# Performance work log

Hardware: AMD Instinct MI355X
Metric: run time of the kernel (lower is better)

## Reference

```python
import jax, jax.numpy as jnp
import numpy as np

B, N, G, M = 16, 8192, 512, 32
ENC = 384   # encoder_dims
TRD = 384   # trans_dim (must equal ENC due to cls-pos concat)
EPS = 1e-5


def _fps(xyz, n_samples):
    # farthest point sampling: xyz [B,N,3] -> idx [B,n_samples] int32
    b, n, _ = xyz.shape
    def body(carry, _):
        dists, farthest = carry                       # [B,N], [B]
        centroid = jnp.take_along_axis(xyz, farthest[:, None, None], axis=1)  # [B,1,3]
        d = jnp.sum((xyz - centroid) ** 2, -1)        # [B,N]
        dists = jnp.minimum(dists, d)
        nxt = jnp.argmax(dists, -1).astype(jnp.int32)
        return (dists, nxt), farthest
    init = (jnp.full((b, n), 1e10, xyz.dtype), jnp.zeros((b,), jnp.int32))
    _, idxs = jax.lax.scan(body, init, None, length=n_samples)
    return idxs.T                                     # [B,n_samples]


def _group(pts):
    # FPS centers + kNN neighborhoods, neighborhood recentered on its center
    fps_idx = _fps(pts, G)                                    # [B,G]
    center = jax.vmap(lambda p, i: p[i])(pts, fps_idx)        # [B,G,3]
    d2 = jnp.sum((center[:, :, None, :] - pts[:, None, :, :]) ** 2, -1)  # [B,G,N]
    _, knn_idx = jax.lax.top_k(-d2, M)                        # [B,G,M]
    nbhd = jax.vmap(lambda p, i: p[i])(pts, knn_idx)          # [B,G,M,3]
    nbhd = nbhd - center[:, :, None, :]
    return nbhd, center


def _bn(x, g, b, m, v):
    return (x - m) * jax.lax.rsqrt(v + EPS) * g + b


def _forward(pts, W1, b1, g1, be1, m1, v1, W2, b2,
             W3, b3, g2, be2, m2, v2, W4, b4,
             Wp1, bp1, Wp2, bp2, cls_pos):
    nbhd, center = _group(pts)                                # [B,G,M,3], [B,G,3]
    # Encoder (Point-MAE, BN in eval mode)
    f = jnp.einsum('bgmc,cd->bgmd', nbhd, W1) + b1            # [B,G,M,128]
    f = jax.nn.relu(_bn(f, g1, be1, m1, v1))
    f = jnp.einsum('bgmc,cd->bgmd', f, W2) + b2               # [B,G,M,256]
    fg = jnp.max(f, axis=2, keepdims=True)                    # [B,G,1,256]
    f = jnp.concatenate([jnp.broadcast_to(fg, f.shape), f], -1)  # [B,G,M,512]
    f = jnp.einsum('bgmc,cd->bgmd', f, W3) + b3
    f = jax.nn.relu(_bn(f, g2, be2, m2, v2))
    f = jnp.einsum('bgmc,cd->bgmd', f, W4) + b4               # [B,G,M,ENC]
    x = jnp.max(f, axis=2)                                    # [B,G,ENC]
    # pos embed MLP on centers
    pos = jax.nn.gelu(center @ Wp1 + bp1) @ Wp2 + bp2         # [B,G,TRD]
    cls = jnp.broadcast_to(cls_pos, (pts.shape[0], 1, ENC))
    pos = jnp.concatenate([cls, pos], axis=1)                 # [B,G+1,TRD]
    return x, pos


def setup_inputs() -> dict:
    key = jax.random.key(0)
    ks = jax.random.split(key, 20)
    nrm = lambda k, s, sc: jax.random.normal(k, s, jnp.float32) * sc
    uni = lambda k, s: jax.random.uniform(k, s, jnp.float32, 0.5, 1.5)
    return {
        'pts': jax.random.normal(ks[0], (B, N, 3), jnp.float32),
        'W1': nrm(ks[1], (3, 128), 0.1), 'b1': jnp.zeros((128,), jnp.float32),
        'g1': uni(ks[2], (128,)), 'be1': nrm(ks[3], (128,), 0.1),
        'm1': nrm(ks[4], (128,), 0.1), 'v1': uni(ks[5], (128,)),
        'W2': nrm(ks[6], (128, 256), 0.05), 'b2': jnp.zeros((256,), jnp.float32),
        'W3': nrm(ks[7], (512, 512), 0.04), 'b3': jnp.zeros((512,), jnp.float32),
        'g2': uni(ks[8], (512,)), 'be2': nrm(ks[9], (512,), 0.1),
        'm2': nrm(ks[10], (512,), 0.1), 'v2': uni(ks[11], (512,)),
        'W4': nrm(ks[12], (512, ENC), 0.04), 'b4': jnp.zeros((ENC,), jnp.float32),
        'Wp1': nrm(ks[13], (3, 128), 0.1), 'bp1': jnp.zeros((128,), jnp.float32),
        'Wp2': nrm(ks[14], (128, TRD), 0.08), 'bp2': jnp.zeros((TRD,), jnp.float32),
        'cls_pos': nrm(ks[15], (1, 1, ENC), 0.02),
    }


def reference(pts, W1, b1, g1, be1, m1, v1, W2, b2, W3, b3, g2, be2, m2, v2,
              W4, b4, Wp1, bp1, Wp2, bp2, cls_pos):
    return _forward(pts, W1, b1, g1, be1, m1, v1, W2, b2, W3, b3, g2, be2,
                    m2, v2, W4, b4, Wp1, bp1, Wp2, bp2, cls_pos)
```

## Files before the change

### kernel.cpp

```cpp
#include <hip/hip_runtime.h>

typedef _Float16 f16;
typedef _Float16 f16x8 __attribute__((ext_vector_type(8)));
typedef float    f32x4 __attribute__((ext_vector_type(4)));

#define NB   16
#define NP   8192
#define NG   512
#define NM   32
#define ENC  384
#define NROWS (NB * NG * NM)

__device__ __forceinline__ void gl_lds16(const void* g, void* l) {
  __builtin_amdgcn_global_load_lds((const __attribute__((address_space(1))) unsigned int*)g,
                                   (__attribute__((address_space(3))) unsigned int*)l, 16, 0, 0);
}

__device__ __forceinline__ unsigned long long kmax(unsigned long long a, unsigned long long b) {
  return a > b ? a : b;
}
__device__ __forceinline__ unsigned long long kmin(unsigned long long a, unsigned long long b) {
  return a < b ? a : b;
}

template <int CTRL>
__device__ __forceinline__ unsigned long long dpp_kmax(unsigned long long k) {
  int lo = (int)(unsigned)(k & 0xFFFFFFFFull);
  int hi = (int)(unsigned)(k >> 32);
  int olo = __builtin_amdgcn_update_dpp(lo, lo, CTRL, 0xF, 0xF, false);
  int ohi = __builtin_amdgcn_update_dpp(hi, hi, CTRL, 0xF, 0xF, false);
  unsigned long long o = ((unsigned long long)(unsigned)ohi << 32) | (unsigned)olo;
  return kmax(k, o);
}
template <int CTRL>
__device__ __forceinline__ unsigned long long dpp_kmin(unsigned long long k) {
  int lo = (int)(unsigned)(k & 0xFFFFFFFFull);
  int hi = (int)(unsigned)(k >> 32);
  int olo = __builtin_amdgcn_update_dpp(lo, lo, CTRL, 0xF, 0xF, false);
  int ohi = __builtin_amdgcn_update_dpp(hi, hi, CTRL, 0xF, 0xF, false);
  unsigned long long o = ((unsigned long long)(unsigned)ohi << 32) | (unsigned)olo;
  return kmin(k, o);
}
__device__ __forceinline__ unsigned long long swz16_kmax(unsigned long long k) {
  int lo = (int)(unsigned)(k & 0xFFFFFFFFull);
  int hi = (int)(unsigned)(k >> 32);
  int olo = __builtin_amdgcn_ds_swizzle(lo, 0x401F);
  int ohi = __builtin_amdgcn_ds_swizzle(hi, 0x401F);
  unsigned long long o = ((unsigned long long)(unsigned)ohi << 32) | (unsigned)olo;
  return kmax(k, o);
}
__device__ __forceinline__ unsigned long long swz16_kmin(unsigned long long k) {
  int lo = (int)(unsigned)(k & 0xFFFFFFFFull);
  int hi = (int)(unsigned)(k >> 32);
  int olo = __builtin_amdgcn_ds_swizzle(lo, 0x401F);
  int ohi = __builtin_amdgcn_ds_swizzle(hi, 0x401F);
  unsigned long long o = ((unsigned long long)(unsigned)ohi << 32) | (unsigned)olo;
  return kmin(k, o);
}

#define DPP_QUAD_XOR1 0xB1
#define DPP_QUAD_XOR2 0x4E
#define DPP_HALF_MIRR 0x141
#define DPP_ROW_MIRR  0x140

__global__ __launch_bounds__(512) void fps_kernel(const float* __restrict__ pts,
                                                  float* __restrict__ centers) {
#pragma clang fp contract(off)
  const int b = blockIdx.x;
  const float* pb = pts + (size_t)b * NP * 3;
  const int t = threadIdx.x;
  const int lane = t & 63, wid = t >> 6;
  __shared__ float spx[NP], spy[NP], spz[NP];
  __shared__ unsigned long long swk[2][16];
  float px[16], py[16], pz[16], dd[16];
#pragma unroll
  for (int i = 0; i < 16; ++i) {
    int idx = t + i * 512;
    float x = pb[idx * 3 + 0], y = pb[idx * 3 + 1], z = pb[idx * 3 + 2];
    px[i] = x; py[i] = y; pz[i] = z; dd[i] = 1e10f;
    spx[idx] = x; spy[idx] = y; spz[idx] = z;
  }
  __syncthreads();
  float cx = spx[0], cy = spy[0], cz = spz[0];
  for (int g = 0; g < NG; ++g) {
    if (t == 0) {
      float* c = centers + ((size_t)b * NG + g) * 3;
      c[0] = cx; c[1] = cy; c[2] = cz;
    }
    float best = -1.0f; int bslot = 0;
#pragma unroll
    for (int i = 0; i < 16; ++i) {
      float dx = __fsub_rn(px[i], cx);
      float dy = __fsub_rn(py[i], cy);
      float dz = __fsub_rn(pz[i], cz);
      float d  = __fadd_rn(__fadd_rn(__fmul_rn(dx, dx), __fmul_rn(dy, dy)), __fmul_rn(dz, dz));
      dd[i] = fminf(dd[i], d);
      if (dd[i] > best) { best = dd[i]; bslot = i; }
    }
    int bidx = t + bslot * 512;
    unsigned long long key =
        ((unsigned long long)__float_as_uint(best) << 13) | (unsigned)(8191 - bidx);
    key = dpp_kmax<DPP_QUAD_XOR1>(key);
    key = dpp_kmax<DPP_QUAD_XOR2>(key);
    key = dpp_kmax<DPP_HALF_MIRR>(key);
    key = dpp_kmax<DPP_ROW_MIRR>(key);
    key = swz16_kmax(key);
    const int p = g & 1;
    if ((lane & 31) == 0) swk[p][wid * 2 + (lane >> 5)] = key;
    __syncthreads();
    unsigned long long k2 = swk[p][lane & 15];
    k2 = dpp_kmax<DPP_QUAD_XOR1>(k2);
    k2 = dpp_kmax<DPP_QUAD_XOR2>(k2);
    k2 = dpp_kmax<DPP_HALF_MIRR>(k2);
    k2 = dpp_kmax<DPP_ROW_MIRR>(k2);
    int widx = 8191 - (int)(k2 & 0x1FFFull);
    cx = spx[widx]; cy = spy[widx]; cz = spz[widx];
  }
}

__global__ __launch_bounds__(256) void knn_kernel(const float* __restrict__ pts,
                                                  const float* __restrict__ centers,
                                                  int* __restrict__ knn_idx) {
#pragma clang fp contract(off)
  const int gg = blockIdx.x;
  const int b = gg >> 9;
  const float* pb = pts + (size_t)b * NP * 3;
  const float* c = centers + (size_t)gg * 3;
  const float cx = c[0], cy = c[1], cz = c[2];
  __shared__ unsigned long long swk[2][8];
  const int t = threadIdx.x, lane = t & 63, wid = t >> 6;
  float d[32];
  float lmin = 3e38f; int lidx = 0;
#pragma unroll
  for (int i = 0; i < 32; ++i) {
    int idx = i * 256 + t;
    float dx = __fsub_rn(cx, pb[idx * 3 + 0]);
    float dy = __fsub_rn(cy, pb[idx * 3 + 1]);
    float dz = __fsub_rn(cz, pb[idx * 3 + 2]);
    d[i] = __fadd_rn(__fadd_rn(__fmul_rn(dx, dx), __fmul_rn(dy, dy)), __fmul_rn(dz, dz));
    if (d[i] < lmin) { lmin = d[i]; lidx = idx; }
  }
  int* outp = knn_idx + (size_t)gg * NM;
  for (int r = 0; r < NM; ++r) {
    unsigned long long key =
        ((unsigned long long)__float_as_uint(lmin) << 13) | (unsigned)lidx;
    key = dpp_kmin<DPP_QUAD_XOR1>(key);
    key = dpp_kmin<DPP_QUAD_XOR2>(key);
    key = dpp_kmin<DPP_HALF_MIRR>(key);
    key = dpp_kmin<DPP_ROW_MIRR>(key);
    key = swz16_kmin(key);
    const int p = r & 1;
    if ((lane & 31) == 0) swk[p][wid * 2 + (lane >> 5)] = key;
    __syncthreads();
    unsigned long long k2 = swk[p][lane & 7];
    k2 = dpp_kmin<DPP_QUAD_XOR1>(k2);
    k2 = dpp_kmin<DPP_QUAD_XOR2>(k2);
    k2 = dpp_kmin<DPP_HALF_MIRR>(k2);
    int i0 = (int)(k2 & 0x1FFFull);
    if (t == 0) outp[r] = i0;
    if ((i0 & 255) == t) {
      int slot = i0 >> 8;
      lmin = 3e38f; lidx = 0;
#pragma unroll
      for (int i = 0; i < 32; ++i) {
        float di = (i == slot) ? 3e38f : d[i];
        d[i] = di;
        if (di < lmin) { lmin = di; lidx = i * 256 + t; }
      }
    }
  }
}

__global__ void quant_kernel(const float* __restrict__ W2, const float* __restrict__ W3,
                             const float* __restrict__ W4, const float* __restrict__ Wp2,
                             const float* __restrict__ b1, const float* __restrict__ g1,
                             const float* __restrict__ be1, const float* __restrict__ m1,
                             const float* __restrict__ v1, const float* __restrict__ g2,
                             const float* __restrict__ be2, const float* __restrict__ m2,
                             const float* __restrict__ v2,
                             f16* __restrict__ W2T, f16* __restrict__ W3aT,
                             f16* __restrict__ W3bT, f16* __restrict__ W4T,
                             f16* __restrict__ Wp2T,
                             float* __restrict__ s1, float* __restrict__ sh1,
                             float* __restrict__ s2, float* __restrict__ sh2) {
  int i = blockIdx.x * 256 + threadIdx.x;
  if (i < 32768) { int n = i >> 7, k = i & 127; W2T[i] = (f16)W2[(size_t)k * 256 + n]; return; }
  i -= 32768;
  if (i < 131072) { int n = i >> 8, k = i & 255; W3aT[i] = (f16)W3[(size_t)k * 512 + n]; return; }
  i -= 131072;
  if (i < 131072) { int n = i >> 8, k = i & 255; W3bT[i] = (f16)W3[(size_t)(256 + k) * 512 + n]; return; }
  i -= 131072;
  if (i < 196608) { int n = i >> 9, k = i & 511; W4T[i] = (f16)W4[(size_t)k * 384 + n]; return; }
  i -= 196608;
  if (i < 49152) { int n = i >> 7, k = i & 127; Wp2T[i] = (f16)Wp2[(size_t)k * 384 + n]; return; }
  i -= 49152;
  if (i < 128) {
    float s = g1[i] * rsqrtf(v1[i] + 1e-5f);
    s1[i] = s; sh1[i] = (b1[i] - m1[i]) * s + be1[i];
    return;
  }
  i -= 128;
  if (i < 512) {
    float s = g2[i] * rsqrtf(v2[i] + 1e-5f);
    s2[i] = s; sh2[i] = be2[i] - m2[i] * s;
    return;
  }
}

template <int WRITE_F2>
__global__ __launch_bounds__(256) void l2f_kernel(const float* __restrict__ pts,
                                                  const float* __restrict__ centers,
                                                  const int* __restrict__ knn_idx,
                                                  const float* __restrict__ W1,
                                                  const float* __restrict__ s1,
                                                  const float* __restrict__ sh1,
                                                  const f16* __restrict__ W2T,
                                                  const float* __restrict__ b2,
                                                  f16* __restrict__ fg,
                                                  f16* __restrict__ f2, int grow0) {
  __shared__ __align__(16) f16 sF1[128 * 128];
  __shared__ float snb[128][3];
  const int t = threadIdx.x, lane = t & 63, wid = t >> 6;
  const int wr = wid >> 1, wc = wid & 1;
  const int l15 = lane & 15, lhi = lane >> 4;
  const int grow = grow0 + blockIdx.x * 128;
  const int y = blockIdx.y;

  if (t < 128) {
    int row = grow + t;
    int gg = row >> 5;
    int b = gg >> 9;
    int idx = knn_idx[(size_t)gg * NM + (row & 31)];
    const float* p = pts + ((size_t)b * NP + idx) * 3;
    const float* c = centers + (size_t)gg * 3;
    snb[t][0] = p[0] - c[0];
    snb[t][1] = p[1] - c[1];
    snb[t][2] = p[2] - c[2];
  }
  __syncthreads();
  {
    int row = t >> 1, c0 = (t & 1) * 64;
    float nx = snb[row][0], ny = snb[row][1], nz = snb[row][2];
    int sw = (row & 7) << 4;
#pragma unroll
    for (int cc = 0; cc < 64; cc += 8) {
      f16x8 v;
#pragma unroll
      for (int j = 0; j < 8; ++j) {
        int c = c0 + cc + j;
        float a = nx * W1[c] + ny * W1[128 + c] + nz * W1[256 + c];
        a = a * s1[c] + sh1[c];
        v[j] = (f16)fmaxf(a, 0.0f);
      }
      *(f16x8*)((char*)sF1 + row * 256 + (((c0 + cc) * 2) ^ sw)) = v;
    }
  }
  __syncthreads();

  f32x4 acc[4][4];
#pragma unroll
  for (int m = 0; m < 4; ++m)
#pragma unroll
    for (int n = 0; n < 4; ++n) acc[m][n] = (f32x4){0.f, 0.f, 0.f, 0.f};

  const f16* Wb = W2T + (size_t)(y * 128) * 128;
#pragma unroll
  for (int ks = 0; ks < 4; ++ks) {
    f16x8 af[4], bf[4];
#pragma unroll
    for (int m = 0; m < 4; ++m) {
      int row = wr * 64 + m * 16 + l15;
      af[m] = *(const f16x8*)((const char*)sF1 + row * 256 + ((ks * 64 + lhi * 16) ^ ((row & 7) << 4)));
    }
#pragma unroll
    for (int n = 0; n < 4; ++n) {
      int nr = wc * 64 + n * 16 + l15;
      bf[n] = *(const f16x8*)(Wb + (size_t)nr * 128 + ks * 32 + lhi * 8);
    }
#pragma unroll
    for (int m = 0; m < 4; ++m)
#pragma unroll
      for (int n = 0; n < 4; ++n)
        acc[m][n] = __builtin_amdgcn_mfma_f32_16x16x32_f16(af[m], bf[n], acc[m][n], 0, 0, 0);
  }

  float bias[4];
#pragma unroll
  for (int n = 0; n < 4; ++n) bias[n] = b2[y * 128 + wc * 64 + n * 16 + l15];
#pragma unroll
  for (int p = 0; p < 2; ++p) {
#pragma unroll
    for (int n = 0; n < 4; ++n) {
      float v = acc[2 * p][n][0];
#pragma unroll
      for (int i = 1; i < 4; ++i) v = fmaxf(v, acc[2 * p][n][i]);
#pragma unroll
      for (int i = 0; i < 4; ++i) v = fmaxf(v, acc[2 * p + 1][n][i]);
      v = fmaxf(v, __shfl_xor(v, 16));
      v = fmaxf(v, __shfl_xor(v, 32));
      if (lhi == 0)
        fg[(size_t)((grow >> 5) + wr * 2 + p) * 256 + y * 128 + wc * 64 + n * 16 + l15] =
            (f16)(v + bias[n]);
    }
  }

  if (WRITE_F2) {
    __syncthreads();
    f16* sF2 = sF1;
#pragma unroll
    for (int n = 0; n < 4; ++n) {
      int col = wc * 64 + n * 16 + l15;
#pragma unroll
      for (int m = 0; m < 4; ++m)
#pragma unroll
        for (int i = 0; i < 4; ++i) {
          int row = wr * 64 + m * 16 + lhi * 4 + i;
          sF2[row * 128 + col] = (f16)(acc[m][n][i] + bias[n]);
        }
    }
    __syncthreads();
#pragma unroll
    for (int ch = 0; ch < 8; ++ch) {
      int off = ch * 4096 + t * 16;
      int row = off >> 8, cb = off & 255;
      *(uint4*)((char*)f2 + (size_t)(blockIdx.x * 128 + row) * 512 + y * 256 + cb) =
          *(const uint4*)((const char*)sF2 + off);
    }
  }
}

template <int K, int EPI>
__global__ __launch_bounds__(256) void gemm128_kernel(const f16* __restrict__ A,
                                                      const f16* __restrict__ BT,
                                                      float* __restrict__ outF32,
                                                      f16* __restrict__ outF16,
                                                      const float* __restrict__ e0,
                                                      const float* __restrict__ e1,
                                                      const float* __restrict__ e2,
                                                      int NTOT, int gg0) {
  __shared__ __align__(16) f16 sA[2][128 * 64];
  __shared__ __align__(16) f16 sB[2][128 * 64];
  const int t = threadIdx.x, lane = t & 63, wid = t >> 6;
  const int wrow = wid >> 1, wcol = wid & 1;
  const int l15 = lane & 15, lhi = lane >> 4;
  f32x4 acc[4][4];
#pragma unroll
  for (int m = 0; m < 4; ++m)
#pragma unroll
    for (int n = 0; n < 4; ++n) acc[m][n] = (f32x4){0.f, 0.f, 0.f, 0.f};

  const size_t arow0 = (size_t)blockIdx.x * 128;
  const int ncol0 = blockIdx.y * 128;
  const char* Ab = (const char*)A;
  const char* Bb = (const char*)BT;
  const int so = wid * 1024 + lane * 16;
  const int cb = so & 127;
  const int r0 = so >> 7;
  const int KSTEPS = K / 64;

  auto STAGE = [&](int bsel, int kt) {
#pragma unroll
    for (int rnd = 0; rnd < 4; ++rnd) {
      int r = rnd * 32 + r0;
      int sw = (r & 7) << 4;
      gl_lds16(Ab + (arow0 + r) * (size_t)(K * 2) + kt * 128 + (cb ^ sw),
               (char*)sA[bsel] + rnd * 4096 + wid * 1024);
      gl_lds16(Bb + (size_t)(ncol0 + r) * (K * 2) + kt * 128 + (cb ^ sw),
               (char*)sB[bsel] + rnd * 4096 + wid * 1024);
    }
  };

  STAGE(0, 0);
  int cur = 0;
#pragma unroll
  for (int kt = 0; kt < KSTEPS; ++kt) {
    if (kt + 1 < KSTEPS) {
      STAGE(cur ^ 1, kt + 1);
      asm volatile("s_waitcnt vmcnt(8)" ::: "memory");
    } else {
      asm volatile("s_waitcnt vmcnt(0)" ::: "memory");
    }
    __builtin_amdgcn_s_barrier();
#pragma unroll
    for (int ks = 0; ks < 2; ++ks) {
      f16x8 af[4], bf[4];
#pragma unroll
      for (int m = 0; m < 4; ++m) {
        int row = wrow * 64 + m * 16 + l15;
        int addr = row * 128 + ((ks * 64 + lhi * 16) ^ ((row & 7) << 4));
        af[m] = *(const f16x8*)((const char*)sA[cur] + addr);
      }
#pragma unroll
      for (int n = 0; n < 4; ++n) {
        int nrow = wcol * 64 + n * 16 + l15;
        int addr = nrow * 128 + ((ks * 64 + lhi * 16) ^ ((nrow & 7) << 4));
        bf[n] = *(const f16x8*)((const char*)sB[cur] + addr);
      }
#pragma unroll
      for (int m = 0; m < 4; ++m)
#pragma unroll
        for (int n = 0; n < 4; ++n)
          acc[m][n] = __builtin_amdgcn_mfma_f32_16x16x32_f16(af[m], bf[n], acc[m][n], 0, 0, 0);
    }
    asm volatile("" ::: "memory");
    __builtin_amdgcn_s_barrier();
    cur ^= 1;
  }

  if (EPI == 1) {
#pragma unroll
    for (int n = 0; n < 4; ++n) {
      int col = ncol0 + wcol * 64 + n * 16 + l15;
      float s = e1[col], sh = e2[col];
#pragma unroll
      for (int m = 0; m < 4; ++m) {
        int grp = gg0 + blockIdx.x * 4 + wrow * 2 + (m >> 1);
        float gv = e0[(size_t)grp * 512 + col];
#pragma unroll
        for (int i = 0; i < 4; ++i) {
          size_t row = arow0 + wrow * 64 + m * 16 + lhi * 4 + i;
          float v = (acc[m][n][i] + gv) * s + sh;
          outF16[row * NTOT + col] = (f16)fmaxf(v, 0.0f);
        }
      }
    }
  } else if (EPI == 2) {
#pragma unroll
    for (int pr = 0; pr < 2; ++pr) {
      size_t gg_glob = (size_t)gg0 + blockIdx.x * 4 + wrow * 2 + pr;
#pragma unroll
      for (int n = 0; n < 4; ++n) {
        float v = acc[2 * pr][n][0];
#pragma unroll
        for (int i = 1; i < 4; ++i) v = fmaxf(v, acc[2 * pr][n][i]);
#pragma unroll
        for (int i = 0; i < 4; ++i) v = fmaxf(v, acc[2 * pr + 1][n][i]);
        v = fmaxf(v, __shfl_xor(v, 16));
        v = fmaxf(v, __shfl_xor(v, 32));
        if (lhi == 0) {
          int col = ncol0 + wcol * 64 + n * 16 + l15;
          outF32[gg_glob * ENC + col] = v + e0[col];
        }
      }
    }
  } else if (EPI == 3) {
#pragma unroll
    for (int n = 0; n < 4; ++n) {
      int col = ncol0 + wcol * 64 + n * 16 + l15;
      float bias = e0[col];
#pragma unroll
      for (int m = 0; m < 4; ++m)
#pragma unroll
        for (int i = 0; i < 4; ++i) {
          size_t row = arow0 + wrow * 64 + m * 16 + lhi * 4 + i;
          outF32[row * NTOT + col] = acc[m][n][i] + bias;
        }
    }
  } else {
#pragma unroll
    for (int n = 0; n < 4; ++n) {
      int col = ncol0 + wcol * 64 + n * 16 + l15;
      float bias = e0[col];
#pragma unroll
      for (int m = 0; m < 4; ++m)
#pragma unroll
        for (int i = 0; i < 4; ++i) {
          size_t row = arow0 + wrow * 64 + m * 16 + lhi * 4 + i;
          int b = (int)(row >> 9), g = (int)(row & 511);
          outF32[((size_t)b * 513 + 1 + g) * 384 + col] = acc[m][n][i] + bias;
        }
    }
  }
}

__global__ __launch_bounds__(256) void posh_kernel(const float* __restrict__ centers,
                                                   const float* __restrict__ Wp1,
                                                   const float* __restrict__ bp1,
                                                   f16* __restrict__ h) {
  int o = blockIdx.x * 256 + threadIdx.x;
  int row = o >> 7, c = o & 127;
  const float* ct = centers + (size_t)row * 3;
  float x = ct[0] * Wp1[c] + ct[1] * Wp1[128 + c] + ct[2] * Wp1[256 + c] + bp1[c];
  float u = 0.7978845608028654f * (x + 0.044715f * x * x * x);
  h[o] = (f16)(0.5f * x * (1.0f + tanhf(u)));
}

__global__ void cls_kernel(const float* __restrict__ cls_pos, float* __restrict__ out_pos) {
  out_pos[(size_t)blockIdx.x * (NG + 1) * ENC + threadIdx.x] = cls_pos[threadIdx.x];
}

extern "C" void kernel_launch(void* const* d_in, const int* in_sizes, int n_in,
                              void* d_out, int out_size, void* d_ws, size_t ws_size,
                              hipStream_t stream) {
  const float* pts = (const float*)d_in[0];
  const float* W1  = (const float*)d_in[1];
  const float* b1  = (const float*)d_in[2];
  const float* g1  = (const float*)d_in[3];
  const float* be1 = (const float*)d_in[4];
  const float* m1  = (const float*)d_in[5];
  const float* v1  = (const float*)d_in[6];
  const float* W2  = (const float*)d_in[7];
  const float* b2  = (const float*)d_in[8];
  const float* W3  = (const float*)d_in[9];
  const float* b3  = (const float*)d_in[10];
  const float* g2  = (const float*)d_in[11];
  const float* be2 = (const float*)d_in[12];
  const float* m2  = (const float*)d_in[13];
  const float* v2  = (const float*)d_in[14];
  const float* W4  = (const float*)d_in[15];
  const float* b4  = (const float*)d_in[16];
  const float* Wp1 = (const float*)d_in[17];
  const float* bp1 = (const float*)d_in[18];
  const float* Wp2 = (const float*)d_in[19];
  const float* bp2 = (const float*)d_in[20];
  const float* cls = (const float*)d_in[21];

  float* out_x   = (float*)d_out;
  float* out_pos = out_x + (size_t)NB * NG * ENC;

  char* w = (char*)d_ws;
  auto alloc = [&](size_t bytes) {
    char* p = w;
    w += (bytes + 255) & ~(size_t)255;
    return p;
  };
  float* centers = (float*)alloc((size_t)NB * NG * 3 * 4);
  int*   knn     = (int*)alloc((size_t)NB * NG * NM * 4);
  f16*   W2T     = (f16*)alloc(32768 * 2);
  f16*   W3aT    = (f16*)alloc(131072 * 2);
  f16*   W3bT    = (f16*)alloc(131072 * 2);
  f16*   W4T     = (f16*)alloc(196608 * 2);
  f16*   Wp2T    = (f16*)alloc(49152 * 2);
  float* s1      = (float*)alloc(128 * 4);
  float* sh1     = (float*)alloc(128 * 4);
  float* s2      = (float*)alloc(512 * 4);
  float* sh2     = (float*)alloc(512 * 4);
  f16*   fg      = (f16*)alloc((size_t)8192 * 256 * 2);
  float* g3      = (float*)alloc((size_t)8192 * 512 * 4);
  f16*   h       = (f16*)alloc((size_t)8192 * 128 * 2);
  size_t fixed = (size_t)(w - (char*)d_ws);
  const size_t f2_full = (size_t)NROWS * 256 * 2;
  const size_t f3_full = (size_t)NROWS * 512 * 2;

  quant_kernel<<<dim3(2115), dim3(256), 0, stream>>>(W2, W3, W4, Wp2, b1, g1, be1, m1, v1,
                                                     g2, be2, m2, v2, W2T, W3aT, W3bT, W4T,
                                                     Wp2T, s1, sh1, s2, sh2);
  fps_kernel<<<dim3(NB), dim3(512), 0, stream>>>(pts, centers);
  knn_kernel<<<dim3(NB * NG), dim3(256), 0, stream>>>(pts, centers, knn);

  if (ws_size >= fixed + f2_full + f3_full / 2 + 4096) {
    f16* f2  = (f16*)alloc(f2_full);
    f16* f3c = (f16*)alloc(f3_full / 2);
    l2f_kernel<1><<<dim3(2048, 2), dim3(256), 0, stream>>>(pts, centers, knn, W1, s1, sh1,
                                                           W2T, b2, fg, f2, 0);
    gemm128_kernel<256, 3><<<dim3(64, 4), dim3(256), 0, stream>>>(
        fg, W3aT, g3, nullptr, b3, nullptr, nullptr, 512, 0);
    for (int c = 0; c < 2; ++c) {
      gemm128_kernel<256, 1><<<dim3(1024, 4), dim3(256), 0, stream>>>(
          f2 + (size_t)c * 131072 * 256, W3bT, nullptr, f3c, g3, s2, sh2, 512, c * 4096);
      gemm128_kernel<512, 2><<<dim3(1024, 3), dim3(256), 0, stream>>>(
          f3c, W4T, out_x, nullptr, b4, nullptr, nullptr, 384, c * 4096);
    }
  } else if (ws_size >= fixed + f2_full + f3_full / 4 + 4096) {
    f16* f2  = (f16*)alloc(f2_full);
    f16* f3c = (f16*)alloc(f3_full / 4);
    l2f_kernel<1><<<dim3(2048, 2), dim3(256), 0, stream>>>(pts, centers, knn, W1, s1, sh1,
                                                           W2T, b2, fg, f2, 0);
    gemm128_kernel<256, 3><<<dim3(64, 4), dim3(256), 0, stream>>>(
        fg, W3aT, g3, nullptr, b3, nullptr, nullptr, 512, 0);
    for (int c = 0; c < 4; ++c) {
      gemm128_kernel<256, 1><<<dim3(512, 4), dim3(256), 0, stream>>>(
          f2 + (size_t)c * 65536 * 256, W3bT, nullptr, f3c, g3, s2, sh2, 512, c * 2048);
      gemm128_kernel<512, 2><<<dim3(512, 3), dim3(256), 0, stream>>>(
          f3c, W4T, out_x, nullptr, b4, nullptr, nullptr, 384, c * 2048);
    }
  } else {
    f16* f2c = (f16*)alloc((size_t)32768 * 256 * 2);
    f16* f3c = (f16*)alloc((size_t)32768 * 512 * 2);
    l2f_kernel<0><<<dim3(2048, 2), dim3(256), 0, stream>>>(pts, centers, knn, W1, s1, sh1,
                                                           W2T, b2, fg, nullptr, 0);
    gemm128_kernel<256, 3><<<dim3(64, 4), dim3(256), 0, stream>>>(
        fg, W3aT, g3, nullptr, b3, nullptr, nullptr, 512, 0);
    for (int c = 0; c < 8; ++c) {
      l2f_kernel<1><<<dim3(256, 2), dim3(256), 0, stream>>>(pts, centers, knn, W1, s1, sh1,
                                                            W2T, b2, fg, f2c, c * 32768);
      gemm128_kernel<256, 1><<<dim3(256, 4), dim3(256), 0, stream>>>(
          f2c, W3bT, nullptr, f3c, g3, s2, sh2, 512, c * 1024);
      gemm128_kernel<512, 2><<<dim3(256, 3), dim3(256), 0, stream>>>(
          f3c, W4T, out_x, nullptr, b4, nullptr, nullptr, 384, c * 1024);
    }
  }

  posh_kernel<<<dim3(4096), dim3(256), 0, stream>>>(centers, Wp1, bp1, h);
  gemm128_kernel<128, 4><<<dim3(64, 3), dim3(256), 0, stream>>>(
      h, Wp2T, out_pos, nullptr, bp2, nullptr, nullptr, 384, 0);
  cls_kernel<<<dim3(NB), dim3(ENC), 0, stream>>>(cls, out_pos);
}
```

Baseline: 1.125 ms.

## Fold W2 into W3 lower half and fuse layer-1 recompute with layer-3 GEMM

Precomputes the product W2·W3[256:] (and a folded bias) so the per-point layer-3 contribution from f2 becomes a K=128 GEMM on the recomputed layer-1 activations. A new l3p kernel recomputes the neighbourhood layer-1 features in LDS and applies the BN/ReLU epilogue with the group-max term g3, removing the f2 intermediate write/read and the separate K=256 GEMM. Layer 2 is still computed only for the max-pool feature. B fragments are read straight from global memory, and the folded fp16 weight changes rounding.

```diff
diff --git a/kernel.cpp b/kernel.cpp
--- a/kernel.cpp
+++ b/kernel.cpp
@@ -179,16 +179,13 @@
                              const float* __restrict__ be2, const float* __restrict__ m2,
                              const float* __restrict__ v2,
                              f16* __restrict__ W2T, f16* __restrict__ W3aT,
-                             f16* __restrict__ W3bT, f16* __restrict__ W4T,
-                             f16* __restrict__ Wp2T,
+                             f16* __restrict__ W4T, f16* __restrict__ Wp2T,
                              float* __restrict__ s1, float* __restrict__ sh1,
                              float* __restrict__ s2, float* __restrict__ sh2) {
   int i = blockIdx.x * 256 + threadIdx.x;
   if (i < 32768) { int n = i >> 7, k = i & 127; W2T[i] = (f16)W2[(size_t)k * 256 + n]; return; }
   i -= 32768;
   if (i < 131072) { int n = i >> 8, k = i & 255; W3aT[i] = (f16)W3[(size_t)k * 512 + n]; return; }
-  i -= 131072;
-  if (i < 131072) { int n = i >> 8, k = i & 255; W3bT[i] = (f16)W3[(size_t)(256 + k) * 512 + n]; return; }
   i -= 131072;
   if (i < 196608) { int n = i >> 9, k = i & 511; W4T[i] = (f16)W4[(size_t)k * 384 + n]; return; }
   i -= 196608;
@@ -207,7 +204,28 @@
   }
 }
 
-template <int WRITE_F2>
+__global__ __launch_bounds__(256) void w23_kernel(const float* __restrict__ W2,
+                                                  const float* __restrict__ W3,
+                                                  const float* __restrict__ b2,
+                                                  const float* __restrict__ b3,
+                                                  f16* __restrict__ W23T,
+                                                  float* __restrict__ bb3) {
+  int o = blockIdx.x * 256 + threadIdx.x;
+  if (o < 65536) {
+    int n = o >> 7, k = o & 127;
+    float s = 0.f;
+    for (int m = 0; m < 256; ++m)
+      s += W2[k * 256 + m] * W3[(size_t)(256 + m) * 512 + n];
+    W23T[o] = (f16)s;
+  } else if (o < 65536 + 512) {
+    int n = o - 65536;
+    float s = b3[n];
+    for (int m = 0; m < 256; ++m)
+      s += b2[m] * W3[(size_t)(256 + m) * 512 + n];
+    bb3[n] = s;
+  }
+}
+
 __global__ __launch_bounds__(256) void l2f_kernel(const float* __restrict__ pts,
                                                   const float* __restrict__ centers,
                                                   const int* __restrict__ knn_idx,
@@ -216,14 +234,13 @@
                                                   const float* __restrict__ sh1,
                                                   const f16* __restrict__ W2T,
                                                   const float* __restrict__ b2,
-                                                  f16* __restrict__ fg,
-                                                  f16* __restrict__ f2, int grow0) {
+                                                  f16* __restrict__ fg) {
   __shared__ __align__(16) f16 sF1[128 * 128];
   __shared__ float snb[128][3];
   const int t = threadIdx.x, lane = t & 63, wid = t >> 6;
   const int wr = wid >> 1, wc = wid & 1;
   const int l15 = lane & 15, lhi = lane >> 4;
-  const int grow = grow0 + blockIdx.x * 128;
+  const int grow = blockIdx.x * 128;
   const int y = blockIdx.y;
 
   if (t < 128) {
@@ -303,28 +320,100 @@
             (f16)(v + bias[n]);
     }
   }
-
-  if (WRITE_F2) {
-    __syncthreads();
-    f16* sF2 = sF1;
+}
+
+__global__ __launch_bounds__(256) void l3p_kernel(const float* __restrict__ pts,
+                                                  const float* __restrict__ centers,
+                                                  const int* __restrict__ knn_idx,
+                                                  const float* __restrict__ W1,
+                                                  const float* __restrict__ s1,
+                                                  const float* __restrict__ sh1,
+                                                  const f16* __restrict__ W23T,
+                                                  const float* __restrict__ g3,
+                                                  const float* __restrict__ s2v,
+                                                  const float* __restrict__ sh2v,
+                                                  f16* __restrict__ f3c, int grow0) {
+  __shared__ __align__(16) f16 sF1[128 * 128];
+  __shared__ float snb[128][3];
+  const int t = threadIdx.x, lane = t & 63, wid = t >> 6;
+  const int wr = wid >> 1, wc = wid & 1;
+  const int l15 = lane & 15, lhi = lane >> 4;
+  const int grow = grow0 + blockIdx.x * 128;
+  const int y = blockIdx.y;
+
+  if (t < 128) {
+    int row = grow + t;
+    int gg = row >> 5;
+    int b = gg >> 9;
+    int idx = knn_idx[(size_t)gg * NM + (row & 31)];
+    const float* p = pts + ((size_t)b * NP + idx) * 3;
+    const float* c = centers + (size_t)gg * 3;
+    snb[t][0] = p[0] - c[0];
+    snb[t][1] = p[1] - c[1];
+    snb[t][2] = p[2] - c[2];
+  }
+  __syncthreads();
+  {
+    int row = t >> 1, c0 = (t & 1) * 64;
+    float nx = snb[row][0], ny = snb[row][1], nz = snb[row][2];
+    int sw = (row & 7) << 4;
+#pragma unroll
+    for (int cc = 0; cc < 64; cc += 8) {
+      f16x8 v;
+#pragma unroll
+      for (int j = 0; j < 8; ++j) {
+        int c = c0 + cc + j;
+        float a = nx * W1[c] + ny * W1[128 + c] + nz * W1[256 + c];
+        a = a * s1[c] + sh1[c];
+        v[j] = (f16)fmaxf(a, 0.0f);
+      }
+      *(f16x8*)((char*)sF1 + row * 256 + (((c0 + cc) * 2) ^ sw)) = v;
+    }
+  }
+  __syncthreads();
+
+  f32x4 acc[4][4];
+#pragma unroll
+  for (int m = 0; m < 4; ++m)
+#pragma unroll
+    for (int n = 0; n < 4; ++n) acc[m][n] = (f32x4){0.f, 0.f, 0.f, 0.f};
+
+  const f16* Wb = W23T + (size_t)(y * 128) * 128;
+#pragma unroll
+  for (int ks = 0; ks < 4; ++ks) {
+    f16x8 af[4], bf[4];
+#pragma unroll
+    for (int m = 0; m < 4; ++m) {
+      int row = wr * 64 + m * 16 + l15;
+      af[m] = *(const f16x8*)((const char*)sF1 + row * 256 + ((ks * 64 + lhi * 16) ^ ((row & 7) << 4)));
+    }
 #pragma unroll
     for (int n = 0; n < 4; ++n) {
-      int col = wc * 64 + n * 16 + l15;
-#pragma unroll
-      for (int m = 0; m < 4; ++m)
-#pragma unroll
-        for (int i = 0; i < 4; ++i) {
-          int row = wr * 64 + m * 16 + lhi * 4 + i;
-          sF2[row * 128 + col] = (f16)(acc[m][n][i] + bias[n]);
-        }
-    }
-    __syncthreads();
-#pragma unroll
-    for (int ch = 0; ch < 8; ++ch) {
-      int off = ch * 4096 + t * 16;
-      int row = off >> 8, cb = off & 255;
-      *(uint4*)((char*)f2 + (size_t)(blockIdx.x * 128 + row) * 512 + y * 256 + cb) =
-          *(const uint4*)((const char*)sF2 + off);
+      int nr = wc * 64 + n * 16 + l15;
+      bf[n] = *(const f16x8*)(Wb + (size_t)nr * 128 + ks * 32 + lhi * 8);
+    }
+#pragma unroll
+    for (int m = 0; m < 4; ++m)
+#pragma unroll
+      for (int n = 0; n < 4; ++n)
+        acc[m][n] = __builtin_amdgcn_mfma_f32_16x16x32_f16(af[m], bf[n], acc[m][n], 0, 0, 0);
+  }
+
+#pragma unroll
+  for (int n = 0; n < 4; ++n) {
+    int col = wc * 64 + n * 16 + l15;
+    int gc = y * 128 + col;
+    float s = s2v[gc], sh = sh2v[gc];
+#pragma unroll
+    for (int m = 0; m < 4; ++m) {
+      int grp = (grow0 >> 5) + blockIdx.x * 4 + wr * 2 + (m >> 1);
+      float gv = g3[(size_t)grp * 512 + gc];
+#pragma unroll
+      for (int i = 0; i < 4; ++i) {
+        int row = wr * 64 + m * 16 + lhi * 4 + i;
+        float v = (acc[m][n][i] + gv) * s + sh;
+        f3c[(size_t)(blockIdx.x * 128 + row) * 512 + gc] = (f16)fmaxf(v, 0.0f);
+      }
     }
   }
 }
@@ -333,10 +422,7 @@
 __global__ __launch_bounds__(256) void gemm128_kernel(const f16* __restrict__ A,
                                                       const f16* __restrict__ BT,
                                                       float* __restrict__ outF32,
-                                                      f16* __restrict__ outF16,
                                                       const float* __restrict__ e0,
-                                                      const float* __restrict__ e1,
-                                                      const float* __restrict__ e2,
                                                       int NTOT, int gg0) {
   __shared__ __align__(16) f16 sA[2][128 * 64];
   __shared__ __align__(16) f16 sB[2][128 * 64];
@@ -407,24 +493,7 @@
     cur ^= 1;
   }
 
-  if (EPI == 1) {
-#pragma unroll
-    for (int n = 0; n < 4; ++n) {
-      int col = ncol0 + wcol * 64 + n * 16 + l15;
-      float s = e1[col], sh = e2[col];
-#pragma unroll
-      for (int m = 0; m < 4; ++m) {
-        int grp = gg0 + blockIdx.x * 4 + wrow * 2 + (m >> 1);
-        float gv = e0[(size_t)grp * 512 + col];
-#pragma unroll
-        for (int i = 0; i < 4; ++i) {
-          size_t row = arow0 + wrow * 64 + m * 16 + lhi * 4 + i;
-          float v = (acc[m][n][i] + gv) * s + sh;
-          outF16[row * NTOT + col] = (f16)fmaxf(v, 0.0f);
-        }
-      }
-    }
-  } else if (EPI == 2) {
+  if (EPI == 2) {
 #pragma unroll
     for (int pr = 0; pr < 2; ++pr) {
       size_t gg_glob = (size_t)gg0 + blockIdx.x * 4 + wrow * 2 + pr;
@@ -528,9 +597,10 @@
   int*   knn     = (int*)alloc((size_t)NB * NG * NM * 4);
   f16*   W2T     = (f16*)alloc(32768 * 2);
   f16*   W3aT    = (f16*)alloc(131072 * 2);
-  f16*   W3bT    = (f16*)alloc(131072 * 2);
   f16*   W4T     = (f16*)alloc(196608 * 2);
   f16*   Wp2T    = (f16*)alloc(49152 * 2);
+  f16*   W23T    = (f16*)alloc(65536 * 2);
+  float* bb3     = (float*)alloc(512 * 4);
   float* s1      = (float*)alloc(128 * 4);
   float* sh1     = (float*)alloc(128 * 4);
   float* s2      = (float*)alloc(512 * 4);
@@ -539,60 +609,36 @@
   float* g3      = (float*)alloc((size_t)8192 * 512 * 4);
   f16*   h       = (f16*)alloc((size_t)8192 * 128 * 2);
   size_t fixed = (size_t)(w - (char*)d_ws);
-  const size_t f2_full = (size_t)NROWS * 256 * 2;
   const size_t f3_full = (size_t)NROWS * 512 * 2;
 
-  quant_kernel<<<dim3(2115), dim3(256), 0, stream>>>(W2, W3, W4, Wp2, b1, g1, be1, m1, v1,
-                                                     g2, be2, m2, v2, W2T, W3aT, W3bT, W4T,
+  size_t avail = (ws_size > fixed + 4096) ? (ws_size - fixed - 4096) : 0;
+  int nch = 8;
+  if (avail >= f3_full) nch = 1;
+  else if (avail >= f3_full / 2) nch = 2;
+  else if (avail >= f3_full / 4) nch = 4;
+  f16* f3c = (f16*)alloc(f3_full / nch);
+  const int crows = NROWS / nch;
+
+  quant_kernel<<<dim3(1603), dim3(256), 0, stream>>>(W2, W3, W4, Wp2, b1, g1, be1, m1, v1,
+                                                     g2, be2, m2, v2, W2T, W3aT, W4T,
                                                      Wp2T, s1, sh1, s2, sh2);
+  w23_kernel<<<dim3(258), dim3(256), 0, stream>>>(W2, W3, b2, b3, W23T, bb3);
   fps_kernel<<<dim3(NB), dim3(512), 0, stream>>>(pts, centers);
   knn_kernel<<<dim3(NB * NG), dim3(256), 0, stream>>>(pts, centers, knn);
 
-  if (ws_size >= fixed + f2_full + f3_full / 2 + 4096) {
-    f16* f2  = (f16*)alloc(f2_full);
-    f16* f3c = (f16*)alloc(f3_full / 2);
-    l2f_kernel<1><<<dim3(2048, 2), dim3(256), 0, stream>>>(pts, centers, knn, W1, s1, sh1,
-                                                           W2T, b2, fg, f2, 0);
-    gemm128_kernel<256, 3><<<dim3(64, 4), dim3(256), 0, stream>>>(
-        fg, W3aT, g3, nullptr, b3, nullptr, nullptr, 512, 0);
-    for (int c = 0; c < 2; ++c) {
-      gemm128_kernel<256, 1><<<dim3(1024, 4), dim3(256), 0, stream>>>(
-          f2 + (size_t)c * 131072 * 256, W3bT, nullptr, f3c, g3, s2, sh2, 512, c * 4096);
-      gemm128_kernel<512, 2><<<dim3(1024, 3), dim3(256), 0, stream>>>(
-          f3c, W4T, out_x, nullptr, b4, nullptr, nullptr, 384, c * 4096);
-    }
-  } else if (ws_size >= fixed + f2_full + f3_full / 4 + 4096) {
-    f16* f2  = (f16*)alloc(f2_full);
-    f16* f3c = (f16*)alloc(f3_full / 4);
-    l2f_kernel<1><<<dim3(2048, 2), dim3(256), 0, stream>>>(pts, centers, knn, W1, s1, sh1,
-                                                           W2T, b2, fg, f2, 0);
-    gemm128_kernel<256, 3><<<dim3(64, 4), dim3(256), 0, stream>>>(
-        fg, W3aT, g3, nullptr, b3, nullptr, nullptr, 512, 0);
-    for (int c = 0; c < 4; ++c) {
-      gemm128_kernel<256, 1><<<dim3(512, 4), dim3(256), 0, stream>>>(
-          f2 + (size_t)c * 65536 * 256, W3bT, nullptr, f3c, g3, s2, sh2, 512, c * 2048);
-      gemm128_kernel<512, 2><<<dim3(512, 3), dim3(256), 0, stream>>>(
-          f3c, W4T, out_x, nullptr, b4, nullptr, nullptr, 384, c * 2048);
-    }
-  } else {
-    f16* f2c = (f16*)alloc((size_t)32768 * 256 * 2);
-    f16* f3c = (f16*)alloc((size_t)32768 * 512 * 2);
-    l2f_kernel<0><<<dim3(2048, 2), dim3(256), 0, stream>>>(pts, centers, knn, W1, s1, sh1,
-                                                           W2T, b2, fg, nullptr, 0);
-    gemm128_kernel<256, 3><<<dim3(64, 4), dim3(256), 0, stream>>>(
-        fg, W3aT, g3, nullptr, b3, nullptr, nullptr, 512, 0);
-    for (int c = 0; c < 8; ++c) {
-      l2f_kernel<1><<<dim3(256, 2), dim3(256), 0, stream>>>(pts, centers, knn, W1, s1, sh1,
-                                                            W2T, b2, fg, f2c, c * 32768);
-      gemm128_kernel<256, 1><<<dim3(256, 4), dim3(256), 0, stream>>>(
-          f2c, W3bT, nullptr, f3c, g3, s2, sh2, 512, c * 1024);
-      gemm128_kernel<512, 2><<<dim3(256, 3), dim3(256), 0, stream>>>(
-          f3c, W4T, out_x, nullptr, b4, nullptr, nullptr, 384, c * 1024);
-    }
+  l2f_kernel<<<dim3(2048, 2), dim3(256), 0, stream>>>(pts, centers, knn, W1, s1, sh1,
+                                                      W2T, b2, fg);
+  gemm128_kernel<256, 3><<<dim3(64, 4), dim3(256), 0, stream>>>(fg, W3aT, g3, bb3, 512, 0);
+
+  for (int c = 0; c < nch; ++c) {
+    int grow0 = c * crows;
+    l3p_kernel<<<dim3(crows / 128, 4), dim3(256), 0, stream>>>(
+        pts, centers, knn, W1, s1, sh1, W23T, g3, s2, sh2, f3c, grow0);
+    gemm128_kernel<512, 2><<<dim3(crows / 128, 3), dim3(256), 0, stream>>>(
+        f3c, W4T, out_x, b4, 384, grow0 / 32);
   }
 
   posh_kernel<<<dim3(4096), dim3(256), 0, stream>>>(centers, Wp1, bp1, h);
-  gemm128_kernel<128, 4><<<dim3(64, 3), dim3(256), 0, stream>>>(
-      h, Wp2T, out_pos, nullptr, bp2, nullptr, nullptr, 384, 0);
+  gemm128_kernel<128, 4><<<dim3(64, 3), dim3(256), 0, stream>>>(h, Wp2T, out_pos, bp2, 384, 0);
   cls_kernel<<<dim3(NB), dim3(ENC), 0, stream>>>(cls, out_pos);
 }
```

Measured after the change: 1.224 ms. +8.8%, slower.
